# Kernel tuning notes

Measured on AMD Instinct MI355X. Metric: run time of the kernel, lower is better.

The kernel has to match this reference:

```python
import jax, jax.numpy as jnp
import numpy as np

H = 256          # hidden_size
TH_X = 0.05      # delta threshold on inputs
TH_H = 0.05      # delta threshold on hidden state
F_IN = 6         # engineered feature count


def hardswish(v):
    return v * jnp.clip(v + 3.0, 0.0, 6.0) / 6.0


def setup_inputs() -> dict:
    key = jax.random.key(0)
    ks = jax.random.split(key, 6)
    B, T = 32, 4096
    x = jax.random.normal(ks[0], (B, T, 2), dtype=jnp.float32)
    # x2h: Linear(6, 3H, bias=False) -> weight (3H, 6)
    Wx = jax.random.normal(ks[1], (3 * H, F_IN), dtype=jnp.float32) * (1.0 / np.sqrt(F_IN))
    # h2h: Linear(H, 3H, bias=False) -> weight (3H, H)
    Wh = jax.random.normal(ks[2], (3 * H, H), dtype=jnp.float32) * (1.0 / np.sqrt(H))
    # fc_out: Linear(H, 2, bias=False)
    Wo = jax.random.normal(ks[3], (2, H), dtype=jnp.float32) * (1.0 / np.sqrt(H))
    # tcn conv1: Conv1d(2, 3, k=3, padding=16, dilation=16, bias=False) -> (O,I,K)=(3,2,3)
    Wc1 = jax.random.normal(ks[4], (3, 2, 3), dtype=jnp.float32) * 0.3
    # tcn conv2: Conv1d(3, 2, k=1) -> (2,3,1)
    Wc2 = jax.random.normal(ks[5], (2, 3, 1), dtype=jnp.float32) * 0.3
    return {"x": x, "Wx": Wx, "Wh": Wh, "Wo": Wo, "Wc1": Wc1, "Wc2": Wc2}


def _delta_gru(feats_TBF, Wx, Wh):
    # feats_TBF: (T, B, 6). Initial states are always zeros (the torch module
    # resets them whenever x_p_0 is None, which DeltaGRUModel always passes).
    T, B, F = feats_TBF.shape
    dt = feats_TBF.dtype
    carry0 = (
        jnp.zeros((B, F), dt),        # x_p
        jnp.zeros((B, H), dt),        # h
        jnp.zeros((B, H), dt),        # h_p
        jnp.zeros((B, H), dt),        # dm_nh
        jnp.zeros((B, 3 * H), dt),    # dm
    )

    def step(carry, xt):
        x_p, h, h_p, dm_nh, dm = carry
        dx = xt - x_p
        dh = h - h_p
        dxa = jnp.abs(dx)
        dha = jnp.abs(dh)
        dx = jnp.where(dxa < TH_X, 0.0, dx)
        dh = jnp.where(dha < TH_H, 0.0, dh)
        x_p = jnp.where(dxa >= TH_X, xt, x_p)
        h_p = jnp.where(dha >= TH_H, h, h_p)
        mac_x = dx @ Wx.T + dm          # (B, 3H)
        mac_h = dh @ Wh.T               # (B, 3H)
        mxr, mxz, mxn = jnp.split(mac_x, 3, axis=1)
        mhr, mhz, mhn = jnp.split(mac_h, 3, axis=1)
        dm_r = mxr + mhr
        dm_z = mxz + mhz
        dm_n = mxn
        dm_nh = mhn + dm_nh
        dm = jnp.concatenate([dm_r, dm_z, dm_n], axis=1)
        r = jax.nn.sigmoid(dm_r)
        z = jax.nn.sigmoid(dm_z)
        n = jnp.tanh(dm_n + r * dm_nh)
        h = (1.0 - z) * n + z * h
        return (x_p, h, h_p, dm_nh, dm), h

    _, hs = jax.lax.scan(step, carry0, feats_TBF)  # hs: (T, B, H)
    return hs


def reference(x, Wx, Wh, Wo, Wc1, Wc2):
    # x: (B, T, 2)
    B, T, _ = x.shape
    # --- TCN skip path ---
    xc = jnp.transpose(x, (0, 2, 1))  # (B, 2, T)
    c1 = jax.lax.conv_general_dilated(
        xc, Wc1, window_strides=(1,), padding=[(16, 16)], rhs_dilation=(16,),
        dimension_numbers=("NCH", "OIH", "NCH"))
    c2 = jax.lax.conv_general_dilated(
        hardswish(c1), Wc2, window_strides=(1,), padding=[(0, 0)],
        dimension_numbers=("NCH", "OIH", "NCH"))
    skip = jnp.transpose(hardswish(c2), (0, 2, 1))  # (B, T, 2)
    # --- engineered features ---
    i = x[..., 0:1]
    q = x[..., 1:2]
    amp2 = i * i + q * q
    amp = jnp.sqrt(jnp.maximum(amp2, 1e-12))
    amp3 = amp * amp2
    i_prev = jnp.pad(i[:, :-1, :], ((0, 0), (1, 0), (0, 0)))
    q_prev = jnp.pad(q[:, :-1, :], ((0, 0), (1, 0), (0, 0)))
    feats = jnp.concatenate([i, q, amp, amp3, i_prev, q_prev], axis=-1)  # (B,T,6)
    # --- delta-GRU scan (time-major) ---
    hs = _delta_gru(jnp.transpose(feats, (1, 0, 2)), Wx, Wh)  # (T, B, H)
    out = jnp.transpose(hs, (1, 0, 2))  # (B, T, H)
    return out @ Wo.T + skip  # (B, T, 2)
```

## Files before the change

kernel.cpp:

```cpp
#include <hip/hip_runtime.h>
#include <math.h>

#define HH 256
#define FIN 6
#define TT 4096
#define BB 32
#define TH 0.05f

typedef _Float16 h2 __attribute__((ext_vector_type(2)));
struct H8 { h2 a, b, c, d; };

__device__ __forceinline__ float hswish(float v) {
    float c = fminf(fmaxf(v + 3.0f, 0.0f), 6.0f);
    return v * c * (1.0f / 6.0f);
}
__device__ __forceinline__ float fexp2(float x) { return __builtin_amdgcn_exp2f(x); }
__device__ __forceinline__ float frcp(float x)  { return __builtin_amdgcn_rcpf(x); }
__device__ __forceinline__ float sigm(float x)  { return frcp(1.0f + fexp2(-1.44269504f * x)); }
__device__ __forceinline__ float tanhf_fast(float x) {
    float ax = fabsf(x);
    float e = fexp2(2.88539008f * ax);
    float t = 1.0f - 2.0f * frcp(e + 1.0f);
    return copysignf(t, x);
}

__global__ __launch_bounds__(256) void k_prep(
        const float* __restrict__ x, const float* __restrict__ Wc1,
        const float* __restrict__ Wc2, float* __restrict__ feats,
        float* __restrict__ out) {
    int idx = blockIdx.x * 256 + threadIdx.x;
    if (idx >= BB * TT) return;
    int b = idx >> 12;
    int t = idx & (TT - 1);
    const float* xb = x + (size_t)b * TT * 2;
    float i0 = xb[t * 2 + 0], q0 = xb[t * 2 + 1];
    float ip = (t > 0) ? xb[(t - 1) * 2 + 0] : 0.0f;
    float qp = (t > 0) ? xb[(t - 1) * 2 + 1] : 0.0f;
    float amp2 = i0 * i0 + q0 * q0;
    float amp  = sqrtf(fmaxf(amp2, 1e-12f));
    float amp3 = amp * amp2;
    float* f = feats + (size_t)idx * 6;
    f[0] = i0; f[1] = q0; f[2] = amp; f[3] = amp3; f[4] = ip; f[5] = qp;

    float c1[3];
#pragma unroll
    for (int m = 0; m < 3; m++) {
        float acc = 0.0f;
#pragma unroll
        for (int k = 0; k < 3; k++) {
            int tt = t + (k - 1) * 16;
            if (tt >= 0 && tt < TT) {
                acc += Wc1[m * 6 + 0 * 3 + k] * xb[tt * 2 + 0];
                acc += Wc1[m * 6 + 1 * 3 + k] * xb[tt * 2 + 1];
            }
        }
        c1[m] = hswish(acc);
    }
#pragma unroll
    for (int o = 0; o < 2; o++) {
        float acc = Wc2[o * 3 + 0] * c1[0] + Wc2[o * 3 + 1] * c1[1] + Wc2[o * 3 + 2] * c1[2];
        out[(size_t)idx * 2 + o] = hswish(acc);
    }
}

__global__ __launch_bounds__(512, 2) void k_gru(
        const float* __restrict__ feats, const float* __restrict__ Wx,
        const float* __restrict__ Wh, const float* __restrict__ Wo,
        float* __restrict__ out) {
    __shared__ float s_out[TT * 2];
    __shared__ __align__(16) _Float16 s_dhh[2][HH];
    __shared__ __align__(16) float s_dx[2][8];
    __shared__ float s_feat[2][128 * FIN];

    const int tid  = threadIdx.x;
    const int wv   = tid >> 6;
    const int lane = tid & 63;
    const int half = lane >> 5;
    const int row  = wv * 32 + (lane & 31);
    const int b    = blockIdx.x;
    const float* fb = feats + (size_t)b * TT * FIN;

    for (int i = tid; i < TT * 2; i += 512) s_out[i] = 0.0f;
    for (int i = tid; i < 128 * FIN; i += 512) s_feat[0][i] = fb[i];

    h2 wr[64], wz[64], wn[64];
    {
        const int k0 = half * 128;
        const float4* p0 = (const float4*)(Wh + (size_t)(0 * HH + row) * HH + k0);
        const float4* p1 = (const float4*)(Wh + (size_t)(1 * HH + row) * HH + k0);
        const float4* p2 = (const float4*)(Wh + (size_t)(2 * HH + row) * HH + k0);
#pragma unroll
        for (int c = 0; c < 32; c++) {
            float4 v0 = p0[c], v1 = p1[c], v2 = p2[c];
            wr[2 * c]     = h2{(_Float16)v0.x, (_Float16)v0.y};
            wr[2 * c + 1] = h2{(_Float16)v0.z, (_Float16)v0.w};
            wz[2 * c]     = h2{(_Float16)v1.x, (_Float16)v1.y};
            wz[2 * c + 1] = h2{(_Float16)v1.z, (_Float16)v1.w};
            wn[2 * c]     = h2{(_Float16)v2.x, (_Float16)v2.y};
            wn[2 * c + 1] = h2{(_Float16)v2.z, (_Float16)v2.w};
        }
    }
    float wxr[FIN], wxz[FIN], wxn[FIN];
#pragma unroll
    for (int f = 0; f < FIN; f++) {
        wxr[f] = Wx[(size_t)(0 * HH + row) * FIN + f];
        wxz[f] = Wx[(size_t)(1 * HH + row) * FIN + f];
        wxn[f] = Wx[(size_t)(2 * HH + row) * FIN + f];
    }
    const float woc = Wo[half * HH + row];

    float h = 0.0f, hp = 0.0f, dmr = 0.0f, dmz = 0.0f, dmn = 0.0f, dmnh = 0.0f;
    float xp = 0.0f, curf = 0.0f;
    if (tid < FIN) curf = fb[tid];

    __syncthreads();

    for (int t = 0; t < TT; t++) {
        const int tb = t & 1;

        if ((t & 127) == 64 && t + 64 < TT) {
            const int w = (t >> 7) + 1;
            for (int i = tid; i < 128 * FIN; i += 512)
                s_feat[w & 1][i] = fb[(size_t)w * 128 * FIN + i];
        }

        {
            float dh = h - hp;
            bool keep = fabsf(dh) >= TH;
            if (half == 0) s_dhh[tb][row] = (_Float16)(keep ? dh : 0.0f);
            if (keep) hp = h;
        }
        if (tid < FIN) {
            float dx = curf - xp;
            bool keep = fabsf(dx) >= TH;
            s_dx[tb][tid] = keep ? dx : 0.0f;
            if (keep) xp = curf;
        }
        __syncthreads();

        float mxr = dmr, mxz = dmz, mxn = dmn;
        {
            const float4* dx4 = (const float4*)s_dx[tb];
            float4 da = dx4[0], db = dx4[1];
            mxr = fmaf(da.x, wxr[0], mxr); mxz = fmaf(da.x, wxz[0], mxz); mxn = fmaf(da.x, wxn[0], mxn);
            mxr = fmaf(da.y, wxr[1], mxr); mxz = fmaf(da.y, wxz[1], mxz); mxn = fmaf(da.y, wxn[1], mxn);
            mxr = fmaf(da.z, wxr[2], mxr); mxz = fmaf(da.z, wxz[2], mxz); mxn = fmaf(da.z, wxn[2], mxn);
            mxr = fmaf(da.w, wxr[3], mxr); mxz = fmaf(da.w, wxz[3], mxz); mxn = fmaf(da.w, wxn[3], mxn);
            mxr = fmaf(db.x, wxr[4], mxr); mxz = fmaf(db.x, wxz[4], mxz); mxn = fmaf(db.x, wxn[4], mxn);
            mxr = fmaf(db.y, wxr[5], mxr); mxz = fmaf(db.y, wxz[5], mxz); mxn = fmaf(db.y, wxn[5], mxn);
        }
        float ar = 0.0f, az = 0.0f, an = 0.0f;
        {
            const H8* dp = (const H8*)s_dhh[tb] + half * 16;
#pragma unroll
            for (int c = 0; c < 16; c++) {
                H8 d = dp[c];
                ar = __builtin_amdgcn_fdot2(d.a, wr[4 * c + 0], ar, false);
                az = __builtin_amdgcn_fdot2(d.a, wz[4 * c + 0], az, false);
                an = __builtin_amdgcn_fdot2(d.a, wn[4 * c + 0], an, false);
                ar = __builtin_amdgcn_fdot2(d.b, wr[4 * c + 1], ar, false);
                az = __builtin_amdgcn_fdot2(d.b, wz[4 * c + 1], az, false);
                an = __builtin_amdgcn_fdot2(d.b, wn[4 * c + 1], an, false);
                ar = __builtin_amdgcn_fdot2(d.c, wr[4 * c + 2], ar, false);
                az = __builtin_amdgcn_fdot2(d.c, wz[4 * c + 2], az, false);
                an = __builtin_amdgcn_fdot2(d.c, wn[4 * c + 2], an, false);
                ar = __builtin_amdgcn_fdot2(d.d, wr[4 * c + 3], ar, false);
                az = __builtin_amdgcn_fdot2(d.d, wz[4 * c + 3], az, false);
                an = __builtin_amdgcn_fdot2(d.d, wn[4 * c + 3], an, false);
            }
        }
        ar += __shfl_xor(ar, 32, 64);
        az += __shfl_xor(az, 32, 64);
        an += __shfl_xor(an, 32, 64);

        dmr = mxr + ar;
        dmz = mxz + az;
        dmn = mxn;
        dmnh += an;

        {
            float r = sigm(dmr);
            float z = sigm(dmz);
            float nn = tanhf_fast(dmn + r * dmnh);
            h = (1.0f - z) * nn + z * h;
        }

        {
            float p = h * woc;
            p += __shfl_xor(p, 16, 64);
            p += __shfl_xor(p, 8, 64);
            p += __shfl_xor(p, 4, 64);
            p += __shfl_xor(p, 2, 64);
            p += __shfl_xor(p, 1, 64);
            if ((lane & 31) == 0) atomicAdd(&s_out[2 * t + half], p);
        }

        if (tid < FIN && t + 1 < TT) {
            const int tn = t + 1;
            curf = s_feat[(tn >> 7) & 1][(tn & 127) * FIN + tid];
        }
    }

    __syncthreads();
    const size_t outbase = (size_t)b * TT * 2;
    for (int i = tid; i < TT * 2; i += 512) out[outbase + i] += s_out[i];
}

extern "C" void kernel_launch(void* const* d_in, const int* in_sizes, int n_in,
                              void* d_out, int out_size, void* d_ws, size_t ws_size,
                              hipStream_t stream) {
    const float* x   = (const float*)d_in[0];
    const float* Wx  = (const float*)d_in[1];
    const float* Wh  = (const float*)d_in[2];
    const float* Wo  = (const float*)d_in[3];
    const float* Wc1 = (const float*)d_in[4];
    const float* Wc2 = (const float*)d_in[5];
    float* out = (float*)d_out;
    float* feats = (float*)d_ws;

    k_prep<<<(BB * TT + 255) / 256, 256, 0, stream>>>(x, Wc1, Wc2, feats, out);
    k_gru<<<BB, 512, 0, stream>>>(feats, Wx, Wh, Wo, out);
}
```

Baseline: 5.213 ms.

## Split GRU hidden-row dot products across four lanes with 1024-thread blocks

Each recurrent GRU block now runs 1024 threads, with each hidden row split across four 16-lane quarters instead of two halves. This halves the per-thread fp16 dot-product chain and the weight registers, shortening the serial per-timestep latency. The input-projection FMAs are also spread across the quarters, and the output reduction uses DPP row shuffles. The cost is an extra cross-lane shuffle stage per gate and a barrier spanning 16 waves instead of 8.

```diff
diff --git a/kernel.cpp b/kernel.cpp
--- a/kernel.cpp
+++ b/kernel.cpp
@@ -22,6 +22,18 @@
     float e = fexp2(2.88539008f * ax);
     float t = 1.0f - 2.0f * frcp(e + 1.0f);
     return copysignf(t, x);
+}
+
+__device__ __forceinline__ float dpp_row_sum16(float p) {
+    int x = __float_as_int(p);
+    p += __int_as_float(__builtin_amdgcn_update_dpp(0, x, 0x118, 0xF, 0xF, true));
+    x = __float_as_int(p);
+    p += __int_as_float(__builtin_amdgcn_update_dpp(0, x, 0x114, 0xF, 0xF, true));
+    x = __float_as_int(p);
+    p += __int_as_float(__builtin_amdgcn_update_dpp(0, x, 0x112, 0xF, 0xF, true));
+    x = __float_as_int(p);
+    p += __int_as_float(__builtin_amdgcn_update_dpp(0, x, 0x111, 0xF, 0xF, true));
+    return p;
 }
 
 __global__ __launch_bounds__(256) void k_prep(
@@ -63,7 +75,7 @@
     }
 }
 
-__global__ __launch_bounds__(512, 2) void k_gru(
+__global__ __launch_bounds__(1024) void k_gru(
         const float* __restrict__ feats, const float* __restrict__ Wx,
         const float* __restrict__ Wh, const float* __restrict__ Wo,
         float* __restrict__ out) {
@@ -75,22 +87,23 @@
     const int tid  = threadIdx.x;
     const int wv   = tid >> 6;
     const int lane = tid & 63;
-    const int half = lane >> 5;
-    const int row  = wv * 32 + (lane & 31);
+    const int q    = lane >> 4;
+    const int row  = wv * 16 + (lane & 15);
     const int b    = blockIdx.x;
     const float* fb = feats + (size_t)b * TT * FIN;
 
-    for (int i = tid; i < TT * 2; i += 512) s_out[i] = 0.0f;
-    for (int i = tid; i < 128 * FIN; i += 512) s_feat[0][i] = fb[i];
-
-    h2 wr[64], wz[64], wn[64];
+    for (int i = tid; i < TT * 2; i += 1024) s_out[i] = 0.0f;
+    for (int i = tid; i < 128 * FIN; i += 1024) s_feat[0][i] = fb[i];
+    if (tid < 4) s_dx[tid >> 1][6 + (tid & 1)] = 0.0f;
+
+    h2 wr[32], wz[32], wn[32];
     {
-        const int k0 = half * 128;
+        const int k0 = q * 64;
         const float4* p0 = (const float4*)(Wh + (size_t)(0 * HH + row) * HH + k0);
         const float4* p1 = (const float4*)(Wh + (size_t)(1 * HH + row) * HH + k0);
         const float4* p2 = (const float4*)(Wh + (size_t)(2 * HH + row) * HH + k0);
 #pragma unroll
-        for (int c = 0; c < 32; c++) {
+        for (int c = 0; c < 16; c++) {
             float4 v0 = p0[c], v1 = p1[c], v2 = p2[c];
             wr[2 * c]     = h2{(_Float16)v0.x, (_Float16)v0.y};
             wr[2 * c + 1] = h2{(_Float16)v0.z, (_Float16)v0.w};
@@ -100,14 +113,16 @@
             wn[2 * c + 1] = h2{(_Float16)v2.z, (_Float16)v2.w};
         }
     }
-    float wxr[FIN], wxz[FIN], wxn[FIN];
-#pragma unroll
-    for (int f = 0; f < FIN; f++) {
-        wxr[f] = Wx[(size_t)(0 * HH + row) * FIN + f];
-        wxz[f] = Wx[(size_t)(1 * HH + row) * FIN + f];
-        wxn[f] = Wx[(size_t)(2 * HH + row) * FIN + f];
-    }
-    const float woc = Wo[half * HH + row];
+    float wxr0 = 0.0f, wxr1 = 0.0f, wxz0 = 0.0f, wxz1 = 0.0f, wxn0 = 0.0f, wxn1 = 0.0f;
+    if (q < 3) {
+        wxr0 = Wx[(size_t)(0 * HH + row) * FIN + 2 * q];
+        wxr1 = Wx[(size_t)(0 * HH + row) * FIN + 2 * q + 1];
+        wxz0 = Wx[(size_t)(1 * HH + row) * FIN + 2 * q];
+        wxz1 = Wx[(size_t)(1 * HH + row) * FIN + 2 * q + 1];
+        wxn0 = Wx[(size_t)(2 * HH + row) * FIN + 2 * q];
+        wxn1 = Wx[(size_t)(2 * HH + row) * FIN + 2 * q + 1];
+    }
+    const float woc = (q < 2) ? Wo[q * HH + row] : 0.0f;
 
     float h = 0.0f, hp = 0.0f, dmr = 0.0f, dmz = 0.0f, dmn = 0.0f, dmnh = 0.0f;
     float xp = 0.0f, curf = 0.0f;
@@ -120,14 +135,14 @@
 
         if ((t & 127) == 64 && t + 64 < TT) {
             const int w = (t >> 7) + 1;
-            for (int i = tid; i < 128 * FIN; i += 512)
+            for (int i = tid; i < 128 * FIN; i += 1024)
                 s_feat[w & 1][i] = fb[(size_t)w * 128 * FIN + i];
         }
 
         {
             float dh = h - hp;
             bool keep = fabsf(dh) >= TH;
-            if (half == 0) s_dhh[tb][row] = (_Float16)(keep ? dh : 0.0f);
+            if (q == 0) s_dhh[tb][row] = (_Float16)(keep ? dh : 0.0f);
             if (keep) hp = h;
         }
         if (tid < FIN) {
@@ -138,22 +153,18 @@
         }
         __syncthreads();
 
-        float mxr = dmr, mxz = dmz, mxn = dmn;
-        {
-            const float4* dx4 = (const float4*)s_dx[tb];
-            float4 da = dx4[0], db = dx4[1];
-            mxr = fmaf(da.x, wxr[0], mxr); mxz = fmaf(da.x, wxz[0], mxz); mxn = fmaf(da.x, wxn[0], mxn);
-            mxr = fmaf(da.y, wxr[1], mxr); mxz = fmaf(da.y, wxz[1], mxz); mxn = fmaf(da.y, wxn[1], mxn);
-            mxr = fmaf(da.z, wxr[2], mxr); mxz = fmaf(da.z, wxz[2], mxz); mxn = fmaf(da.z, wxn[2], mxn);
-            mxr = fmaf(da.w, wxr[3], mxr); mxz = fmaf(da.w, wxz[3], mxz); mxn = fmaf(da.w, wxn[3], mxn);
-            mxr = fmaf(db.x, wxr[4], mxr); mxz = fmaf(db.x, wxz[4], mxz); mxn = fmaf(db.x, wxn[4], mxn);
-            mxr = fmaf(db.y, wxr[5], mxr); mxz = fmaf(db.y, wxz[5], mxz); mxn = fmaf(db.y, wxn[5], mxn);
-        }
-        float ar = 0.0f, az = 0.0f, an = 0.0f;
-        {
-            const H8* dp = (const H8*)s_dhh[tb] + half * 16;
-#pragma unroll
-            for (int c = 0; c < 16; c++) {
+        float ar, az, an, axn;
+        {
+            const float2 dxp = *((const float2*)s_dx[tb] + q);
+            ar  = fmaf(dxp.x, wxr0, dxp.y * wxr1);
+            az  = fmaf(dxp.x, wxz0, dxp.y * wxz1);
+            axn = fmaf(dxp.x, wxn0, dxp.y * wxn1);
+            an  = 0.0f;
+        }
+        {
+            const H8* dp = (const H8*)s_dhh[tb] + q * 8;
+#pragma unroll
+            for (int c = 0; c < 8; c++) {
                 H8 d = dp[c];
                 ar = __builtin_amdgcn_fdot2(d.a, wr[4 * c + 0], ar, false);
                 az = __builtin_amdgcn_fdot2(d.a, wz[4 * c + 0], az, false);
@@ -169,13 +180,14 @@
                 an = __builtin_amdgcn_fdot2(d.d, wn[4 * c + 3], an, false);
             }
         }
-        ar += __shfl_xor(ar, 32, 64);
-        az += __shfl_xor(az, 32, 64);
-        an += __shfl_xor(an, 32, 64);
-
-        dmr = mxr + ar;
-        dmz = mxz + az;
-        dmn = mxn;
+        ar  += __shfl_xor(ar, 16, 64);  ar  += __shfl_xor(ar, 32, 64);
+        az  += __shfl_xor(az, 16, 64);  az  += __shfl_xor(az, 32, 64);
+        an  += __shfl_xor(an, 16, 64);  an  += __shfl_xor(an, 32, 64);
+        axn += __shfl_xor(axn, 16, 64); axn += __shfl_xor(axn, 32, 64);
+
+        dmr += ar;
+        dmz += az;
+        dmn += axn;
         dmnh += an;
 
         {
@@ -187,12 +199,8 @@
 
         {
             float p = h * woc;
-            p += __shfl_xor(p, 16, 64);
-            p += __shfl_xor(p, 8, 64);
-            p += __shfl_xor(p, 4, 64);
-            p += __shfl_xor(p, 2, 64);
-            p += __shfl_xor(p, 1, 64);
-            if ((lane & 31) == 0) atomicAdd(&s_out[2 * t + half], p);
+            p = dpp_row_sum16(p);
+            if ((lane & 15) == 15 && q < 2) atomicAdd(&s_out[2 * t + q], p);
         }
 
         if (tid < FIN && t + 1 < TT) {
@@ -203,7 +211,7 @@
 
     __syncthreads();
     const size_t outbase = (size_t)b * TT * 2;
-    for (int i = tid; i < TT * 2; i += 512) out[outbase + i] += s_out[i];
+    for (int i = tid; i < TT * 2; i += 1024) out[outbase + i] += s_out[i];
 }
 
 extern "C" void kernel_launch(void* const* d_in, const int* in_sizes, int n_in,
@@ -219,5 +227,5 @@
     float* feats = (float*)d_ws;
 
     k_prep<<<(BB * TT + 255) / 256, 256, 0, stream>>>(x, Wc1, Wc2, feats, out);
-    k_gru<<<BB, 512, 0, stream>>>(feats, Wx, Wh, Wo, out);
-}
+    k_gru<<<BB, 1024, 0, stream>>>(feats, Wx, Wh, Wo, out);
+}
```

After: 6.161 ms. 1.18x slower.
